# Performance work log

Measured on AMD Instinct MI355X. Metric: run time of the kernel, lower is better.

Reference implementation:

```python
import jax, jax.numpy as jnp
import numpy as np
from jax.scipy.special import logsumexp

B, T, D, H, K = 64, 800, 80, 128, 39  # batch, frames, feat dim, LSTM hidden/dir, num phones


def setup_inputs() -> dict:
    key = jax.random.key(0)
    ks = jax.random.split(key, 16)
    s = 0.1
    inp = {
        "features": jax.random.normal(ks[0], (B, T, D), jnp.float32),
        "lengths": jax.random.randint(ks[1], (B,), T // 2, T + 1, dtype=jnp.int32),
        "labels": jax.random.randint(ks[2], (B, T), 0, K, dtype=jnp.int32),
        # BiLSTM params (PyTorch layout: W_ih (4H,D), W_hh (4H,H); gate order i,f,g,o)
        "Wih_f": jax.random.normal(ks[3], (4 * H, D), jnp.float32) * s,
        "Whh_f": jax.random.normal(ks[4], (4 * H, H), jnp.float32) * s,
        "bih_f": jax.random.normal(ks[5], (4 * H,), jnp.float32) * s,
        "bhh_f": jax.random.normal(ks[6], (4 * H,), jnp.float32) * s,
        "Wih_b": jax.random.normal(ks[7], (4 * H, D), jnp.float32) * s,
        "Whh_b": jax.random.normal(ks[8], (4 * H, H), jnp.float32) * s,
        "bih_b": jax.random.normal(ks[9], (4 * H,), jnp.float32) * s,
        "bhh_b": jax.random.normal(ks[10], (4 * H,), jnp.float32) * s,
        # emission projection Linear(2H -> K)
        "Wp": jax.random.normal(ks[11], (K, 2 * H), jnp.float32) * s,
        "bp": jax.random.normal(ks[12], (K,), jnp.float32) * s,
        # CRF params (pytorch-crf init: U(-0.1, 0.1))
        "start_t": jax.random.uniform(ks[13], (K,), jnp.float32, -0.1, 0.1),
        "end_t": jax.random.uniform(ks[14], (K,), jnp.float32, -0.1, 0.1),
        "trans": jax.random.uniform(ks[15], (K, K), jnp.float32, -0.1, 0.1),
    }
    return inp


def _lstm(x, Wih, Whh, bih, bhh, reverse):
    """Single-direction LSTM over padded batch. x: (B,T,D) -> (B,T,H)."""
    nB, nT, _ = x.shape
    nH = Whh.shape[1]
    xW = jnp.swapaxes(x @ Wih.T + (bih + bhh), 0, 1)  # (T,B,4H)

    def step(carry, g):
        h, c = carry
        g = g + h @ Whh.T
        i, f, gg, o = jnp.split(g, 4, axis=-1)
        c = jax.nn.sigmoid(f) * c + jax.nn.sigmoid(i) * jnp.tanh(gg)
        h = jax.nn.sigmoid(o) * jnp.tanh(c)
        return (h, c), h

    init = (jnp.zeros((nB, nH), x.dtype), jnp.zeros((nB, nH), x.dtype))
    _, hs = jax.lax.scan(step, init, xW, reverse=reverse)
    return jnp.swapaxes(hs, 0, 1)  # (B,T,H)


def _crf_nll(emissions, labels, lengths, start_t, end_t, trans):
    """pytorch-crf: -mean log-likelihood. emissions (B,T,K), labels (B,T)."""
    nB, nT, nK = emissions.shape
    mask = (jnp.arange(nT)[None, :] < lengths[:, None])  # (B,T)
    mf = mask.astype(emissions.dtype)
    bidx = jnp.arange(nB)

    # --- numerator: score of gold path ---
    num = start_t[labels[:, 0]] + emissions[bidx, 0, labels[:, 0]]
    tr = trans[labels[:, :-1], labels[:, 1:]]  # (B,T-1)
    em = jnp.take_along_axis(emissions[:, 1:], labels[:, 1:, None], axis=2)[..., 0]
    num = num + ((tr + em) * mf[:, 1:]).sum(axis=1)
    last_tags = jnp.take_along_axis(labels, (lengths - 1)[:, None], axis=1)[:, 0]
    num = num + end_t[last_tags]

    # --- denominator: forward algorithm ---
    alpha0 = start_t[None, :] + emissions[:, 0]  # (B,K)
    em_rest = jnp.swapaxes(emissions[:, 1:], 0, 1)  # (T-1,B,K)
    m_rest = jnp.swapaxes(mask[:, 1:], 0, 1)  # (T-1,B)

    def step(alpha, inputs):
        em_t, m_t = inputs
        nxt = logsumexp(alpha[:, :, None] + trans[None] + em_t[:, None, :], axis=1)
        return jnp.where(m_t[:, None], nxt, alpha), None

    alpha, _ = jax.lax.scan(step, alpha0, (em_rest, m_rest))
    denom = logsumexp(alpha + end_t[None, :], axis=1)

    return -(num - denom).mean()


def reference(features, lengths, labels, Wih_f, Whh_f, bih_f, bhh_f,
              Wih_b, Whh_b, bih_b, bhh_b, Wp, bp, start_t, end_t, trans):
    h_f = _lstm(features, Wih_f, Whh_f, bih_f, bhh_f, reverse=False)
    h_b = _lstm(features, Wih_b, Whh_b, bih_b, bhh_b, reverse=True)
    hidden = jnp.concatenate([h_f, h_b], axis=-1)  # (B,T,2H)
    emissions = hidden @ Wp.T + bp  # (B,T,K)
    return _crf_nll(emissions, labels, lengths, start_t, end_t, trans)
```

## Files before the change

### kernel.cpp

```cpp
#include <hip/hip_runtime.h>
#include <cstddef>
#include <cstdint>

#define B_ 64
#define T_ 800
#define D_ 80
#define H_ 128
#define K_ 39
#define BT_ (B_ * T_)

#define GCH_ 32
#define NCH_ 25
#define CHF_ 1664

#define NL2E_  (-1.44269504f)
#define N2L2E_ (-2.88539008f)
#define L2E_   (1.44269504f)

typedef _Float16 h2_t  __attribute__((ext_vector_type(2)));
typedef _Float16 f16x8 __attribute__((ext_vector_type(8)));
typedef float    f32x4 __attribute__((ext_vector_type(4)));
typedef uint32_t u32x4 __attribute__((ext_vector_type(4)));

__device__ __forceinline__ float fdot2_(h2_t a, h2_t b, float c) {
#if __has_builtin(__builtin_amdgcn_fdot2)
  return __builtin_amdgcn_fdot2(a, b, c, false);
#else
  return c + (float)a.x * (float)b.x + (float)a.y * (float)b.y;
#endif
}

__device__ __forceinline__ h2_t asH2u_(uint32_t u) { return __builtin_bit_cast(h2_t, u); }

__device__ __forceinline__ float ex2_(float x) {
#if __has_builtin(__builtin_amdgcn_exp2f)
  return __builtin_amdgcn_exp2f(x);
#else
  return __builtin_exp2f(x);
#endif
}
__device__ __forceinline__ float rcpf_(float x) {
#if __has_builtin(__builtin_amdgcn_rcpf)
  return __builtin_amdgcn_rcpf(x);
#else
  return 1.0f / x;
#endif
}
__device__ __forceinline__ float tanhf_(float x) { return 2.0f / (1.0f + __expf(-2.0f * x)) - 1.0f; }

__device__ __forceinline__ float laneb_(float v, int lane) {
  return __builtin_bit_cast(float, __builtin_amdgcn_readlane(__builtin_bit_cast(int, v), lane));
}
__device__ __forceinline__ uint32_t lanebu_(uint32_t v, int lane) {
  return (uint32_t)__builtin_amdgcn_readlane((int)v, lane);
}

__device__ __forceinline__ float dppswap1_(float v) {
  return __builtin_bit_cast(float,
    __builtin_amdgcn_mov_dpp(__builtin_bit_cast(int, v), 0xB1, 0xF, 0xF, true));
}

__device__ __forceinline__ void barrier_lds_() {
  asm volatile("s_waitcnt lgkmcnt(0)" ::: "memory");
  __builtin_amdgcn_s_barrier();
}

__device__ __forceinline__ void rows_of_(int tid, int& unit, int& role, int& r0, int& r1) {
  const int w = tid >> 6, L = tid & 63;
  unit = w * 32 + (L >> 1);
  role = L & 1;
  r0 = role * H_ + unit;
  r1 = 2 * H_ + role * H_ + unit;
}

__global__ __launch_bounds__(256, 1)
void xw_kernel(const float* __restrict__ x,
               const float* __restrict__ Wih_f, const float* __restrict__ Wih_b,
               _Float16* __restrict__ xw)
{
  const int dir = blockIdx.x & 1;
  const int mc  = blockIdx.x >> 1;
  const float* W = dir ? Wih_b : Wih_f;

  const int tid  = threadIdx.x;
  const int w    = tid >> 6;
  const int lane = tid & 63;
  const int lm   = lane & 15;
  const int quad = lane >> 4;
  const int selw = w >> 1;
  const int rolw = w & 1;

  f16x8 Bf[8][3];
  #pragma unroll
  for (int nt = 0; nt < 8; ++nt) {
    const int r = w * 128 + nt * 16 + lm;
    const float fac = (r >= 256 && r < 384) ? N2L2E_ : NL2E_;
    #pragma unroll
    for (int kt = 0; kt < 3; ++kt) {
      const int kb = kt * 32 + quad * 8;
      #pragma unroll
      for (int j = 0; j < 8; ++j) {
        const int k = kb + j;
        Bf[nt][kt][j] = (k < D_) ? (_Float16)(fac * W[(size_t)r * D_ + k]) : (_Float16)0.0f;
      }
    }
  }

  __shared__ alignas(16) _Float16 xs[128 * 96];
  __shared__ alignas(16) _Float16 xo[16 * 512];
  for (int i = tid; i < 128 * 96; i += 256) xs[i] = (_Float16)0.0f;

  for (int cc = 0; cc < 4; ++cc) {
    const int base = mc * 512 + cc * 128;
    __syncthreads();
    {
      const float4* src = (const float4*)(x + (size_t)base * D_);
      for (int i = tid; i < 128 * D_ / 4; i += 256) {
        float4 v = src[i];
        const int row = i / 20, col = (i % 20) * 4;
        h2_t p0, p1;
        p0.x = (_Float16)v.x; p0.y = (_Float16)v.y;
        p1.x = (_Float16)v.z; p1.y = (_Float16)v.w;
        uint2 pk;
        pk.x = __builtin_bit_cast(uint32_t, p0);
        pk.y = __builtin_bit_cast(uint32_t, p1);
        *(uint2*)&xs[row * 96 + col] = pk;
      }
    }
    __syncthreads();

    #pragma unroll
    for (int mt = 0; mt < 8; ++mt) {
      f16x8 Af[3];
      #pragma unroll
      for (int kt = 0; kt < 3; ++kt)
        Af[kt] = *(const f16x8*)&xs[(mt * 16 + lm) * 96 + kt * 32 + quad * 8];

      f32x4 acc[8];
      #pragma unroll
      for (int nt = 0; nt < 8; ++nt) acc[nt] = (f32x4){0.f, 0.f, 0.f, 0.f};
      #pragma unroll
      for (int kt = 0; kt < 3; ++kt)
        #pragma unroll
        for (int nt = 0; nt < 8; ++nt)
          acc[nt] = __builtin_amdgcn_mfma_f32_16x16x32_f16(Af[kt], Bf[nt][kt], acc[nt], 0, 0, 0);

      #pragma unroll
      for (int nt = 0; nt < 8; ++nt) {
        const int unit = nt * 16 + lm;
        const int pcol = ((unit >> 5) * 64 + (unit & 31) * 2 + rolw) * 2 + selw;
        #pragma unroll
        for (int rg = 0; rg < 4; ++rg)
          xo[(quad * 4 + rg) * 512 + pcol] = (_Float16)acc[nt][rg];
      }
      __syncthreads();
      {
        const size_t gbase = ((size_t)dir * BT_ + base + mt * 16) * 512;
        const uint4* src4 = (const uint4*)xo;
        uint4* dst4 = (uint4*)(xw + gbase);
        #pragma unroll
        for (int i = 0; i < 4; ++i)
          dst4[tid + i * 256] = src4[tid + i * 256];
      }
      __syncthreads();
    }
  }
}

template<int USE_XW>
__global__ __launch_bounds__(256, 1)
void lstm_kernel(const float* __restrict__ x,
                 const float* __restrict__ Wih_f, const float* __restrict__ Whh_f,
                 const float* __restrict__ bih_f, const float* __restrict__ bhh_f,
                 const float* __restrict__ Wih_b, const float* __restrict__ Whh_b,
                 const float* __restrict__ bih_b, const float* __restrict__ bhh_b,
                 const _Float16* __restrict__ xw,
                 _Float16* __restrict__ hcat)
{
  const int bb  = blockIdx.x & 63;
  const int dir = blockIdx.x >> 6;
  const float* Whh = dir ? Whh_b : Whh_f;
  const float* Wih = dir ? Wih_b : Wih_f;
  const float* bih = dir ? bih_b : bih_f;
  const float* bhh = dir ? bhh_b : bhh_f;

  const int tid  = threadIdx.x;
  const int lane = tid & 63;
  int unit, role, r0, r1; rows_of_(tid, unit, role, r0, r1);
  const float s0 = NL2E_;
  const float s1 = role ? NL2E_ : N2L2E_;
  const float qk2 = role ? 0.0f : -1.0f;

  h2_t w0[64], w1[64];
  #pragma unroll
  for (int j = 0; j < 64; ++j) {
    float2 a = *(const float2*)(Whh + (size_t)r0 * H_ + 2 * j);
    float2 d = *(const float2*)(Whh + (size_t)r1 * H_ + 2 * j);
    w0[j].x = (_Float16)(s0 * a.x); w0[j].y = (_Float16)(s0 * a.y);
    w1[j].x = (_Float16)(s1 * d.x); w1[j].y = (_Float16)(s1 * d.y);
  }
  h2_t wx0[40], wx1[40];
  if (!USE_XW) {
    #pragma unroll
    for (int i = 0; i < 40; ++i) {
      float2 a = *(const float2*)(Wih + (size_t)r0 * D_ + 2 * i);
      float2 d = *(const float2*)(Wih + (size_t)r1 * D_ + 2 * i);
      wx0[i].x = (_Float16)(s0 * a.x); wx0[i].y = (_Float16)(s0 * a.y);
      wx1[i].x = (_Float16)(s1 * d.x); wx1[i].y = (_Float16)(s1 * d.y);
    }
  }
  const float bias0 = s0 * (bih[r0] + bhh[r0]);
  const float bias1 = s1 * (bih[r1] + bhh[r1]);

  __shared__ alignas(16) _Float16 hsf[2][H_];
  __shared__ uint32_t xs2[2][64];

  if (tid < H_) hsf[0][tid] = (_Float16)0.0f;
  if (!USE_XW && tid < 64) { xs2[0][tid] = 0u; xs2[1][tid] = 0u; }
  float c = 0.0f;

  const uint32_t* xwdu = (const uint32_t*)xw + ((size_t)dir * BT_ + (size_t)bb * T_) * 256;
  const float*    xb   = x + (size_t)bb * T_ * D_;
  _Float16*       hb   = hcat + (size_t)bb * T_ * (2 * H_) + dir * H_;

  _Float16* hbp = hb + (size_t)(dir ? (T_ - 1) : 0) * (2 * H_);
  const ptrdiff_t hstep = dir ? -(2 * H_) : (2 * H_);
  int xoff = (dir ? (T_ - 3) : 2) * 256 + tid;
  const int xstep = dir ? -256 : 256;

  uint32_t xwA = 0u, xwB = 0u;
  h2_t xpend; xpend.x = (_Float16)0.f; xpend.y = (_Float16)0.f;
  {
    const int tq0 = dir ? (T_ - 1) : 0;
    const int tq1 = dir ? (T_ - 2) : 1;
    if (USE_XW) {
      xwA = xwdu[(size_t)tq0 * 256 + tid];
      xwB = xwdu[(size_t)tq1 * 256 + tid];
    } else if (tid < 40) {
      float2 v0 = *(const float2*)(xb + (size_t)tq0 * D_ + 2 * tid);
      h2_t p; p.x = (_Float16)v0.x; p.y = (_Float16)v0.y;
      xs2[0][tid] = __builtin_bit_cast(uint32_t, p);
      float2 v1 = *(const float2*)(xb + (size_t)tq1 * D_ + 2 * tid);
      xpend.x = (_Float16)v1.x; xpend.y = (_Float16)v1.y;
    }
  }
  __syncthreads();

  auto step = [&](int tt, int par, uint32_t& xwreg) {
    float a0, a1, a2, a3, b0, b1, b2, b3;
    if (USE_XW) {
      const h2_t xv = asH2u_(xwreg);
      a0 = bias0 + (float)xv.x;
      b0 = bias1 + (float)xv.y;
      a1 = a2 = a3 = 0.f; b1 = b2 = b3 = 0.f;
      xwreg = xwdu[xoff];
    } else {
      a0 = bias0; b0 = bias1;
      a1 = a2 = a3 = 0.f; b1 = b2 = b3 = 0.f;
      if (tid < 40) {
        xs2[par ^ 1][tid] = __builtin_bit_cast(uint32_t, xpend);
        const int ttc = (tt + 2 < T_) ? (tt + 2) : (T_ - 1);
        const int tq2 = dir ? (T_ - 1 - ttc) : ttc;
        float2 v = *(const float2*)(xb + (size_t)tq2 * D_ + 2 * tid);
        xpend.x = (_Float16)v.x; xpend.y = (_Float16)v.y;
      }
      uint32_t xreg = xs2[par][lane];
      #pragma unroll
      for (int j = 0; j < 40; j += 4) {
        h2_t q0 = asH2u_(lanebu_(xreg, j));
        h2_t q1 = asH2u_(lanebu_(xreg, j + 1));
        h2_t q2 = asH2u_(lanebu_(xreg, j + 2));
        h2_t q3 = asH2u_(lanebu_(xreg, j + 3));
        a0 = fdot2_(wx0[j],     q0, a0); b0 = fdot2_(wx1[j],     q0, b0);
        a1 = fdot2_(wx0[j + 1], q1, a1); b1 = fdot2_(wx1[j + 1], q1, b1);
        a2 = fdot2_(wx0[j + 2], q2, a2); b2 = fdot2_(wx1[j + 2], q2, b2);
        a3 = fdot2_(wx0[j + 3], q3, a3); b3 = fdot2_(wx1[j + 3], q3, b3);
      }
    }

    const u32x4* hq = (const u32x4*)hsf[par];
    #pragma unroll
    for (int g = 0; g < 16; ++g) {
      const u32x4 hv = hq[g];
      a0 = fdot2_(w0[4 * g + 0], asH2u_(hv[0]), a0);
      b0 = fdot2_(w1[4 * g + 0], asH2u_(hv[0]), b0);
      a1 = fdot2_(w0[4 * g + 1], asH2u_(hv[1]), a1);
      b1 = fdot2_(w1[4 * g + 1], asH2u_(hv[1]), b1);
      a2 = fdot2_(w0[4 * g + 2], asH2u_(hv[2]), a2);
      b2 = fdot2_(w1[4 * g + 2], asH2u_(hv[2]), b2);
      a3 = fdot2_(w0[4 * g + 3], asH2u_(hv[3]), a3);
      b3 = fdot2_(w1[4 * g + 3], asH2u_(hv[3]), b3);
    }
    const float ga = (a0 + a1) + (a2 + a3);
    const float gb = (b0 + b1) + (b2 + b3);

    const float ea = ex2_(ga);
    const float sg = rcpf_(1.0f + ea);
    const float gbc = fminf(fmaxf(gb, -34.6f), 34.6f);
    const float eb = ex2_(gbc);
    const float qv = fmaf(qk2, eb, 1.0f) * rcpf_(1.0f + eb);
    const float ex = dppswap1_(sg * qv);
    c = fmaf(sg, c, ex);
    const float hn = qv * tanhf_(c);
    if (role) {
      hsf[par ^ 1][unit] = (_Float16)hn;
      hbp[unit] = (_Float16)hn;
    }
    hbp += hstep;
    if (tt + 3 < T_) xoff += xstep;
    barrier_lds_();
  };

  for (int tb = 0; tb < T_; tb += 2) {
    step(tb,     0, xwA);
    step(tb + 1, 1, xwB);
  }
}

__global__ __launch_bounds__(256, 1)
void emis_kernel(const _Float16* __restrict__ hcat,
                 const float* __restrict__ Wp, const float* __restrict__ bp,
                 float* __restrict__ em)
{
  const int tid  = threadIdx.x;
  const int w    = tid >> 6;
  const int lane = tid & 63;
  const int lm   = lane & 15;
  const int quad = lane >> 4;

  f16x8 Bf[3][8];
  float bias[3];
  #pragma unroll
  for (int nt = 0; nt < 3; ++nt) {
    const int n = nt * 16 + lm;
    const bool valid = n < K_;
    bias[nt] = valid ? bp[n] : 0.0f;
    #pragma unroll
    for (int kt = 0; kt < 8; ++kt) {
      const int kb = kt * 32 + quad * 8;
      #pragma unroll
      for (int j = 0; j < 8; ++j)
        Bf[nt][kt][j] = valid ? (_Float16)Wp[(size_t)n * 256 + kb + j] : (_Float16)0.0f;
    }
  }

  #pragma unroll
  for (int q = 0; q < 4; ++q) {
    const int mt  = blockIdx.x * 16 + w * 4 + q;
    const int bt0 = mt * 16;

    f16x8 Af[8];
    const _Float16* ab = hcat + ((size_t)bt0 + lm) * 256;
    #pragma unroll
    for (int kt = 0; kt < 8; ++kt)
      Af[kt] = *(const f16x8*)(ab + kt * 32 + quad * 8);

    f32x4 acc[3];
    #pragma unroll
    for (int nt = 0; nt < 3; ++nt) acc[nt] = (f32x4){0.f, 0.f, 0.f, 0.f};
    #pragma unroll
    for (int kt = 0; kt < 8; ++kt)
      #pragma unroll
      for (int nt = 0; nt < 3; ++nt)
        acc[nt] = __builtin_amdgcn_mfma_f32_16x16x32_f16(Af[kt], Bf[nt][kt], acc[nt], 0, 0, 0);

    #pragma unroll
    for (int nt = 0; nt < 3; ++nt) {
      const int n = nt * 16 + lm;
      if (n < K_) {
        #pragma unroll
        for (int rg = 0; rg < 4; ++rg) {
          const int row = bt0 + quad * 4 + rg;
          em[(size_t)row * K_ + n] = acc[nt][rg] + bias[nt];
        }
      }
    }
  }
}

__global__ __launch_bounds__(64, 1)
void crf_chunk_kernel(const float* __restrict__ em,
                      const int* __restrict__ lengths,
                      const float* __restrict__ trans,
                      float* __restrict__ Pbuf)
{
  const int b    = blockIdx.x / NCH_;
  const int c    = blockIdx.x % NCH_;
  const int lane = threadIdx.x;
  const int lm   = lane & 15;
  const int quad = lane >> 4;
  const int len  = lengths[b];
  const int t0   = 1 + c * GCH_;
  int t1 = 1 + (c + 1) * GCH_;
  if (t1 > T_)  t1 = T_;
  if (t1 > len) t1 = len;

  f16x8 Bf[3][2];
  #pragma unroll
  for (int nt = 0; nt < 3; ++nt) {
    const int n = nt * 16 + lm;
    #pragma unroll
    for (int kf = 0; kf < 2; ++kf) {
      #pragma unroll
      for (int jj = 0; jj < 8; ++jj) {
        const int j = kf * 32 + quad * 8 + jj;
        Bf[nt][kf][jj] = (j < K_ && n < K_)
          ? (_Float16)__expf(trans[j * K_ + n]) : (_Float16)0.0f;
      }
    }
  }

  __shared__ alignas(16) _Float16 Plds[48 * 68];
  for (int i = lane; i < 48 * 68; i += 64) Plds[i] = (_Float16)0.0f;
  if (lane < K_) Plds[lane * 68 + lane] = (_Float16)1.0f;
  asm volatile("s_waitcnt lgkmcnt(0)" ::: "memory");

  float sacc = 0.0f;
  const float* emb = em + (size_t)b * T_ * K_;

  for (int t = t0; t < t1; ++t) {
    float emv[3], e3[3];
    float mloc = -1e30f;
    #pragma unroll
    for (int nt = 0; nt < 3; ++nt) {
      const int col = nt * 16 + lm;
      emv[nt] = (col < K_) ? emb[(size_t)t * K_ + col] : -1e30f;
      mloc = fmaxf(mloc, emv[nt]);
    }
    #pragma unroll
    for (int off = 8; off >= 1; off >>= 1)
      mloc = fmaxf(mloc, __shfl_xor(mloc, off));
    #pragma unroll
    for (int nt = 0; nt < 3; ++nt) {
      const int col = nt * 16 + lm;
      e3[nt] = (col < K_) ? ex2_((emv[nt] - mloc) * L2E_) : 0.0f;
    }

    f32x4 acc[3][3];
    #pragma unroll
    for (int mt = 0; mt < 3; ++mt)
      #pragma unroll
      for (int nt = 0; nt < 3; ++nt)
        acc[mt][nt] = (f32x4){0.f, 0.f, 0.f, 0.f};
    #pragma unroll
    for (int kf = 0; kf < 2; ++kf) {
      f16x8 Am[3];
      #pragma unroll
      for (int mt = 0; mt < 3; ++mt)
        Am[mt] = *(const f16x8*)&Plds[(mt * 16 + lm) * 68 + kf * 32 + quad * 8];
      #pragma unroll
      for (int mt = 0; mt < 3; ++mt)
        #pragma unroll
        for (int nt = 0; nt < 3; ++nt)
          acc[mt][nt] = __builtin_amdgcn_mfma_f32_16x16x32_f16(Am[mt], Bf[nt][kf], acc[mt][nt], 0, 0, 0);
    }

    float sv[3][3][4];
    float mx = 0.0f;
    #pragma unroll
    for (int mt = 0; mt < 3; ++mt)
      #pragma unroll
      for (int nt = 0; nt < 3; ++nt)
        #pragma unroll
        for (int rg = 0; rg < 4; ++rg) {
          const float s = acc[mt][nt][rg] * e3[nt];
          sv[mt][nt][rg] = s;
          mx = fmaxf(mx, s);
        }
    #pragma unroll
    for (int off = 32; off >= 1; off >>= 1)
      mx = fmaxf(mx, __shfl_xor(mx, off));
    const float rmx = rcpf_(mx);
    sacc += mloc - __logf(rmx);

    #pragma unroll
    for (int mt = 0; mt < 3; ++mt)
      #pragma unroll
      for (int nt = 0; nt < 3; ++nt)
        #pragma unroll
        for (int rg = 0; rg < 4; ++rg) {
          const int row = mt * 16 + quad * 4 + rg;
          const int col = nt * 16 + lm;
          Plds[row * 68 + col] = (_Float16)(sv[mt][nt][rg] * rmx);
        }
    asm volatile("s_waitcnt lgkmcnt(0)" ::: "memory");
  }

  float* rec = Pbuf + ((size_t)(b * NCH_ + c)) * CHF_;
  for (int i = lane; i < 1600; i += 64) {
    const int r = i / 40, cc2 = i % 40;
    rec[i] = (float)Plds[r * 68 + cc2];
  }
  if (lane == 0) rec[1600] = sacc;
}

__global__ __launch_bounds__(256)
void crf_comb2_kernel(const float* __restrict__ em,
                      const int* __restrict__ labels, const int* __restrict__ lengths,
                      const float* __restrict__ start_t, const float* __restrict__ end_t,
                      const float* __restrict__ trans,
                      const float* __restrict__ Pbuf,
                      float* __restrict__ dn)
{
  const int b    = blockIdx.x;
  const int tid  = threadIdx.x;
  const int wv   = tid >> 6;
  const int lane = tid & 63;
  const int len  = lengths[b];
  const float* emb = em + (size_t)b * T_ * K_;

  __shared__ float s_num[3];
  __shared__ float s_den;

  if (wv == 0) {
    float a0 = (lane < K_) ? (start_t[lane] + emb[lane]) : -1e30f;
    float m = a0;
    #pragma unroll
    for (int off = 32; off > 0; off >>= 1) m = fmaxf(m, __shfl_xor(m, off));
    float av = __expf(a0 - m);
    float off_acc = m;

    for (int c = 0; c < NCH_; ++c) {
      const float* rec = Pbuf + ((size_t)(b * NCH_ + c)) * CHF_;
      const float pv = av;
      float s0 = 0.f, s1 = 0.f, s2 = 0.f, s3 = 0.f;
      #pragma unroll
      for (int j = 0; j < 36; j += 4) {
        s0 = fmaf(laneb_(pv, j),     rec[(j)     * 40 + lane], s0);
        s1 = fmaf(laneb_(pv, j + 1), rec[(j + 1) * 40 + lane], s1);
        s2 = fmaf(laneb_(pv, j + 2), rec[(j + 2) * 40 + lane], s2);
        s3 = fmaf(laneb_(pv, j + 3), rec[(j + 3) * 40 + lane], s3);
      }
      s0 = fmaf(laneb_(pv, 36), rec[36 * 40 + lane], s0);
      s1 = fmaf(laneb_(pv, 37), rec[37 * 40 + lane], s1);
      s2 = fmaf(laneb_(pv, 38), rec[38 * 40 + lane], s2);
      float vn = (lane < K_) ? ((s0 + s1) + (s2 + s3)) : 0.0f;
      float mx = vn;
      #pragma unroll
      for (int off = 32; off > 0; off >>= 1) mx = fmaxf(mx, __shfl_xor(mx, off));
      const float rmx = rcpf_(mx);
      av = vn * rmx;
      off_acc += rec[1600] - __logf(rmx);
    }

    float w = (lane < K_) ? av * __expf(end_t[lane]) : 0.0f;
    #pragma unroll
    for (int off = 32; off > 0; off >>= 1) w += __shfl_xor(w, off);
    if (lane == 0) s_den = off_acc + __logf(w);
  } else {
    const int idx = tid - 64;
    float acc = 0.0f;
    for (int t = 1 + idx; t < len; t += 192) {
      const int lp = labels[b * T_ + t - 1];
      const int lc = labels[b * T_ + t];
      acc += trans[lp * K_ + lc] + emb[(size_t)t * K_ + lc];
    }
    if (tid == 64) {
      const int l0 = labels[b * T_];
      const int ll = labels[b * T_ + len - 1];
      acc += start_t[l0] + emb[l0] + end_t[ll];
    }
    #pragma unroll
    for (int off = 32; off > 0; off >>= 1) acc += __shfl_xor(acc, off);
    if (lane == 0) s_num[wv - 1] = acc;
  }
  __syncthreads();
  if (tid == 0) dn[b] = s_den - (s_num[0] + s_num[1] + s_num[2]);
}

__global__ __launch_bounds__(256)
void crf_dn_kernel(const float* __restrict__ em,
                   const int* __restrict__ labels, const int* __restrict__ lengths,
                   const float* __restrict__ start_t, const float* __restrict__ end_t,
                   const float* __restrict__ trans,
                   float* __restrict__ dn)
{
  const int b    = blockIdx.x;
  const int tid  = threadIdx.x;
  const int wv   = tid >> 6;
  const int lane = tid & 63;
  const int len  = lengths[b];
  const float* emb = em + (size_t)b * T_ * K_;

  __shared__ float s_num[3];
  __shared__ float s_den;

  if (wv == 0) {
    float et[K_];
    #pragma unroll
    for (int j = 0; j < K_; ++j)
      et[j] = (lane < K_) ? __expf(trans[j * K_ + lane]) : 0.0f;

    float a0 = (lane < K_) ? (start_t[lane] + emb[lane]) : -1e30f;
    float m = a0;
    #pragma unroll
    for (int off = 32; off > 0; off >>= 1) m = fmaxf(m, __shfl_xor(m, off));
    float v = __expf(a0 - m);
    float off_acc = m;

    auto ldc = [&](int t) -> float {
      const int tc = (t < len) ? t : (len - 1);
      return (lane < K_) ? emb[(size_t)tc * K_ + lane] : 0.0f;
    };

    float eA = ldc(1), eB = ldc(2), eC = ldc(3), eD = ldc(4);
    float eE = ldc(5), eF = ldc(6), eG = ldc(7), eH = ldc(8);

    auto stepden = [&](float& ereg, int tt) {
      const float emc = ereg;
      ereg = ldc(tt + 8);
      if (tt < len) {
        const float pv = v;
        float s0 = 0.f, s1 = 0.f, s2 = 0.f, s3 = 0.f;
        #pragma unroll
        for (int j = 0; j < 36; j += 4) {
          s0 = fmaf(laneb_(pv, j),     et[j],     s0);
          s1 = fmaf(laneb_(pv, j + 1), et[j + 1], s1);
          s2 = fmaf(laneb_(pv, j + 2), et[j + 2], s2);
          s3 = fmaf(laneb_(pv, j + 3), et[j + 3], s3);
        }
        s0 = fmaf(laneb_(pv, 36), et[36], s0);
        s1 = fmaf(laneb_(pv, 37), et[37], s1);
        s2 = fmaf(laneb_(pv, 38), et[38], s2);
        v = ((s0 + s1) + (s2 + s3)) * __expf(emc);
        if ((tt & 3) == 0) {
          const float sc = laneb_(v, 0);
          v *= 1.0f / sc;
          off_acc += __logf(sc);
        }
      }
    };

    for (int t = 1; t < len; t += 8) {
      stepden(eA, t);     stepden(eB, t + 1);
      stepden(eC, t + 2); stepden(eD, t + 3);
      stepden(eE, t + 4); stepden(eF, t + 5);
      stepden(eG, t + 6); stepden(eH, t + 7);
    }

    float w = (lane < K_) ? v * __expf(end_t[lane]) : 0.0f;
    #pragma unroll
    for (int off = 32; off > 0; off >>= 1) w += __shfl_xor(w, off);
    if (lane == 0) s_den = off_acc + __logf(w);
  } else {
    const int idx = tid - 64;
    float acc = 0.0f;
    for (int t = 1 + idx; t < len; t += 192) {
      const int lp = labels[b * T_ + t - 1];
      const int lc = labels[b * T_ + t];
      acc += trans[lp * K_ + lc] + emb[(size_t)t * K_ + lc];
    }
    if (tid == 64) {
      const int l0 = labels[b * T_];
      const int ll = labels[b * T_ + len - 1];
      acc += start_t[l0] + emb[l0] + end_t[ll];
    }
    #pragma unroll
    for (int off = 32; off > 0; off >>= 1) acc += __shfl_xor(acc, off);
    if (lane == 0) s_num[wv - 1] = acc;
  }
  __syncthreads();
  if (tid == 0) dn[b] = s_den - (s_num[0] + s_num[1] + s_num[2]);
}

__global__ void finalize_kernel(const float* __restrict__ dn, float* __restrict__ out)
{
  const int tid = threadIdx.x;
  float v = dn[tid];
  #pragma unroll
  for (int off = 32; off > 0; off >>= 1) v += __shfl_down(v, off);
  if (tid == 0) out[0] = v * (1.0f / 64.0f);
}

extern "C" void kernel_launch(void* const* d_in, const int* in_sizes, int n_in,
                              void* d_out, int out_size, void* d_ws, size_t ws_size,
                              hipStream_t stream)
{
  (void)in_sizes; (void)n_in; (void)out_size;
  const float* features = (const float*)d_in[0];
  const int*   lengths  = (const int*)d_in[1];
  const int*   labels   = (const int*)d_in[2];
  const float* Wih_f = (const float*)d_in[3];
  const float* Whh_f = (const float*)d_in[4];
  const float* bih_f = (const float*)d_in[5];
  const float* bhh_f = (const float*)d_in[6];
  const float* Wih_b = (const float*)d_in[7];
  const float* Whh_b = (const float*)d_in[8];
  const float* bih_b = (const float*)d_in[9];
  const float* bhh_b = (const float*)d_in[10];
  const float* Wp      = (const float*)d_in[11];
  const float* bp      = (const float*)d_in[12];
  const float* start_t = (const float*)d_in[13];
  const float* end_t   = (const float*)d_in[14];
  const float* trans   = (const float*)d_in[15];
  float* out = (float*)d_out;

  char* wsc = (char*)d_ws;
  _Float16* hcatH = (_Float16*)wsc;
  float*    em    = (float*)(wsc + 26214400);
  float*    dn    = (float*)(wsc + 26214400 + 7987200);
  _Float16* xwH   = (_Float16*)(wsc + 34202112);
  float*    Pbuf  = (float*)(wsc + 34202112);
  const bool big  = ws_size >= (size_t)34202112 + 104857600;

  if (big) {
    hipLaunchKernelGGL(xw_kernel, dim3(200), dim3(256), 0, stream,
                       features, Wih_f, Wih_b, xwH);
    hipLaunchKernelGGL((lstm_kernel<1>), dim3(2 * B_), dim3(256), 0, stream,
                       features, Wih_f, Whh_f, bih_f, bhh_f,
                       Wih_b, Whh_b, bih_b, bhh_b, xwH, hcatH);
    hipLaunchKernelGGL(emis_kernel, dim3(BT_ / 256), dim3(256), 0, stream,
                       hcatH, Wp, bp, em);
    hipLaunchKernelGGL(crf_chunk_kernel, dim3(B_ * NCH_), dim3(64), 0, stream,
                       em, lengths, trans, Pbuf);
    hipLaunchKernelGGL(crf_comb2_kernel, dim3(B_), dim3(256), 0, stream,
                       em, labels, lengths, start_t, end_t, trans, Pbuf, dn);
  } else {
    hipLaunchKernelGGL((lstm_kernel<0>), dim3(2 * B_), dim3(256), 0, stream,
                       features, Wih_f, Whh_f, bih_f, bhh_f,
                       Wih_b, Whh_b, bih_b, bhh_b, xwH, hcatH);
    hipLaunchKernelGGL(emis_kernel, dim3(BT_ / 256), dim3(256), 0, stream,
                       hcatH, Wp, bp, em);
    hipLaunchKernelGGL(crf_dn_kernel, dim3(B_), dim3(256), 0, stream,
                       em, labels, lengths, start_t, end_t, trans, dn);
  }
  hipLaunchKernelGGL(finalize_kernel, dim3(1), dim3(64), 0, stream,
                     dn, out);
}
```

Before: 639.1 us.

## Fuse emission projection into CRF chunk kernel and drop separate emis launch

Each CRF chunk block now computes its own 32 rows of emissions from the LSTM hidden states with MFMA. It keeps them in shared memory for the chunk recurrence and also writes them to global memory for the combine kernel. Chunk 0 additionally computes the t=0 emission row with a dot-product path. This removes one kernel launch and the global round-trip of emissions before the chunk scan. In exchange, each block loads the full Wp into registers, which raises register pressure and per-block setup work.

New measurement: 670.4 us. 4.9% more time.

```diff
diff --git a/kernel.cpp b/kernel.cpp
--- a/kernel.cpp
+++ b/kernel.cpp
@@ -379,9 +379,11 @@
 }
 
 __global__ __launch_bounds__(64, 1)
-void crf_chunk_kernel(const float* __restrict__ em,
+void crf_chunk_kernel(const _Float16* __restrict__ hcat,
+                      const float* __restrict__ Wp, const float* __restrict__ bp,
                       const int* __restrict__ lengths,
                       const float* __restrict__ trans,
+                      float* __restrict__ em,
                       float* __restrict__ Pbuf)
 {
   const int b    = blockIdx.x / NCH_;
@@ -395,6 +397,22 @@
   if (t1 > T_)  t1 = T_;
   if (t1 > len) t1 = len;
 
+  f16x8 Bp[3][8];
+  float bias[3];
+  #pragma unroll
+  for (int nt = 0; nt < 3; ++nt) {
+    const int n = nt * 16 + lm;
+    const bool valid = n < K_;
+    bias[nt] = valid ? bp[n] : 0.0f;
+    #pragma unroll
+    for (int kt = 0; kt < 8; ++kt) {
+      const int kb = kt * 32 + quad * 8;
+      #pragma unroll
+      for (int j = 0; j < 8; ++j)
+        Bp[nt][kt][j] = valid ? (_Float16)Wp[(size_t)n * 256 + kb + j] : (_Float16)0.0f;
+    }
+  }
+
   f16x8 Bf[3][2];
   #pragma unroll
   for (int nt = 0; nt < 3; ++nt) {
@@ -411,20 +429,71 @@
   }
 
   __shared__ alignas(16) _Float16 Plds[48 * 68];
+  __shared__ alignas(16) float ems[GCH_ * 40];
   for (int i = lane; i < 48 * 68; i += 64) Plds[i] = (_Float16)0.0f;
   if (lane < K_) Plds[lane * 68 + lane] = (_Float16)1.0f;
+
+  #pragma unroll
+  for (int mt2 = 0; mt2 < 2; ++mt2) {
+    const int trow = t0 + mt2 * 16 + lm;
+    const int trc  = (trow < T_) ? trow : (T_ - 1);
+    const _Float16* ar = hcat + ((size_t)b * T_ + trc) * 256;
+    f16x8 Af[8];
+    #pragma unroll
+    for (int kt = 0; kt < 8; ++kt)
+      Af[kt] = *(const f16x8*)(ar + kt * 32 + quad * 8);
+
+    f32x4 acc[3];
+    #pragma unroll
+    for (int nt = 0; nt < 3; ++nt) acc[nt] = (f32x4){0.f, 0.f, 0.f, 0.f};
+    #pragma unroll
+    for (int kt = 0; kt < 8; ++kt)
+      #pragma unroll
+      for (int nt = 0; nt < 3; ++nt)
+        acc[nt] = __builtin_amdgcn_mfma_f32_16x16x32_f16(Af[kt], Bp[nt][kt], acc[nt], 0, 0, 0);
+
+    #pragma unroll
+    for (int nt = 0; nt < 3; ++nt) {
+      const int n = nt * 16 + lm;
+      if (n < K_) {
+        #pragma unroll
+        for (int rg = 0; rg < 4; ++rg) {
+          const int lr = mt2 * 16 + quad * 4 + rg;
+          const int tr = t0 + lr;
+          const float val = acc[nt][rg] + bias[nt];
+          ems[lr * 40 + n] = val;
+          if (tr < T_)
+            em[((size_t)b * T_ + tr) * K_ + n] = val;
+        }
+      }
+    }
+  }
+
+  if (c == 0 && lane < K_) {
+    const h2_t* h0 = (const h2_t*)(hcat + (size_t)b * T_ * 256);
+    const float* wr = Wp + (size_t)lane * 256;
+    float acc = bias[0] * 0.0f + bp[lane];
+    float a1 = 0.f;
+    #pragma unroll
+    for (int k = 0; k < 128; k += 2) {
+      h2_t wpk, wpk1;
+      wpk.x  = (_Float16)wr[2 * k];     wpk.y  = (_Float16)wr[2 * k + 1];
+      wpk1.x = (_Float16)wr[2 * k + 2]; wpk1.y = (_Float16)wr[2 * k + 3];
+      acc = fdot2_(h0[k],     wpk,  acc);
+      a1  = fdot2_(h0[k + 1], wpk1, a1);
+    }
+    em[(size_t)b * T_ * K_ + lane] = acc + a1;
+  }
   asm volatile("s_waitcnt lgkmcnt(0)" ::: "memory");
 
   float sacc = 0.0f;
-  const float* emb = em + (size_t)b * T_ * K_;
-
   for (int t = t0; t < t1; ++t) {
     float emv[3], e3[3];
     float mloc = -1e30f;
     #pragma unroll
     for (int nt = 0; nt < 3; ++nt) {
       const int col = nt * 16 + lm;
-      emv[nt] = (col < K_) ? emb[(size_t)t * K_ + col] : -1e30f;
+      emv[nt] = (col < K_) ? ems[(t - t0) * 40 + col] : -1e30f;
       mloc = fmaxf(mloc, emv[nt]);
     }
     #pragma unroll
@@ -709,10 +778,8 @@
     hipLaunchKernelGGL((lstm_kernel<1>), dim3(2 * B_), dim3(256), 0, stream,
                        features, Wih_f, Whh_f, bih_f, bhh_f,
                        Wih_b, Whh_b, bih_b, bhh_b, xwH, hcatH);
-    hipLaunchKernelGGL(emis_kernel, dim3(BT_ / 256), dim3(256), 0, stream,
-                       hcatH, Wp, bp, em);
     hipLaunchKernelGGL(crf_chunk_kernel, dim3(B_ * NCH_), dim3(64), 0, stream,
-                       em, lengths, trans, Pbuf);
+                       hcatH, Wp, bp, lengths, trans, em, Pbuf);
     hipLaunchKernelGGL(crf_comb2_kernel, dim3(B_), dim3(256), 0, stream,
                        em, labels, lengths, start_t, end_t, trans, Pbuf, dn);
   } else {
```
